# Kernel optimization log

Measured on AMD Instinct MI355X. Metric: run time of the kernel, lower is better.

## Reference

```python
import jax, jax.numpy as jnp
import numpy as np
import math

LMAX = 8
NUM_VECTORS = 64
N_COEF = (LMAX + 1) * (LMAX + 2) // 2  # 45 even-order SH coefficients


def _dfact(n):
    out = 1.0
    k = n
    while k > 1:
        out *= k
        k -= 2
    return out


def sh_tournier_all(xyz, lmax=LMAX):
    """Real even-order spherical harmonics, orders 0,2,...,lmax concatenated
    (m = -l..l within each order), with the Tournier (-1)^|m| sign applied and
    the input permuted xyz -> yzx and normalized (as in the torch module).
    Output: xyz.shape[:-1] + (45,). Fully polynomial in the unit vector, so it
    is smooth/differentiable (no atan2 / division by sin(theta))."""
    yzx = xyz[..., jnp.array([1, 2, 0])]
    r = jnp.sqrt(jnp.sum(yzx * yzx, axis=-1, keepdims=True) + 1e-12)
    u = yzx / r
    px, py, pz = u[..., 0], u[..., 1], u[..., 2]
    # A_m = rho^m cos(m*phi), B_m = rho^m sin(m*phi) via Chebyshev-style recurrence
    A = [jnp.ones_like(px)]
    Bv = [jnp.zeros_like(px)]
    for m in range(1, lmax + 1):
        A.append(px * A[-1] - py * Bv[-1])
        Bv.append(px * Bv[-1] + py * A[-2])
    # Q[l,m] = P_l^m / sin^m(theta): polynomial in pz (Condon-Shortley included)
    Q = {}
    for m in range(lmax + 1):
        qmm = ((-1.0) ** m) * _dfact(2 * m - 1)
        Q[(m, m)] = jnp.full_like(pz, qmm)
        if m < lmax:
            Q[(m + 1, m)] = (2 * m + 1) * qmm * pz
        for l in range(m + 2, lmax + 1):
            Q[(l, m)] = ((2 * l - 1) * pz * Q[(l - 1, m)]
                         - (l + m - 1) * Q[(l - 2, m)]) / (l - m)
    blocks = []
    sqrt2 = math.sqrt(2.0)
    for l in range(0, lmax + 1, 2):
        comps = []
        for m in range(-l, l + 1):
            am = abs(m)
            K = math.sqrt((2 * l + 1) / (4 * math.pi)
                          * math.factorial(l - am) / math.factorial(l + am))
            sgn = -1.0 if am % 2 == 1 else 1.0  # Tournier normalization sign
            if m < 0:
                val = sqrt2 * K * Q[(l, am)] * Bv[am]
            elif m == 0:
                val = K * Q[(l, 0)]
            else:
                val = sqrt2 * K * Q[(l, am)] * A[am]
            comps.append(sgn * val)
        blocks.append(jnp.stack(comps, axis=-1))
    return jnp.concatenate(blocks, axis=-1)


def _forward(image, affine, psf_vectors, M_p):
    B, X, Y, Z, C = image.shape
    V = psf_vectors.shape[0]
    img = jnp.transpose(image.reshape(B, -1, C), (0, 2, 1))      # [B,C,N]
    affine_inv = jnp.linalg.inv(affine)                           # [B,X,Y,Z,3,3]
    w = jnp.einsum('vc,bcn->bvn', M_p, img)                       # PSF weights [B,V,N]
    vi = psf_vectors.T                                            # [3,V]
    vi_hat = affine_inv @ vi                                      # [B,X,Y,Z,3,V]
    M_prime = sh_tournier_all(jnp.swapaxes(vi_hat, -1, -2))       # [B,X,Y,Z,V,C]
    # modulation: |A^{-1} v| / det(A^{-1}) per voxel per vector
    mod = (jnp.sqrt(jnp.sum(vi_hat * vi_hat, axis=-2))
           / jnp.linalg.det(affine_inv)[..., None])               # [B,X,Y,Z,V]
    mod = jnp.moveaxis(mod, -1, 1).reshape(B, V, -1)              # [B,V,N]
    w_mod = mod * w                                               # [B,V,N]
    # per-voxel small GEMV: out[b,n,c] = sum_v M_prime[b,n,v,c] * w_mod[b,v,n]
    out = jnp.einsum('bnvc,bvn->bnc', M_prime.reshape(B, -1, V, C), w_mod)
    return out.reshape(image.shape)


def setup_inputs() -> dict:
    key = jax.random.key(0)
    k1, k2, k3 = jax.random.split(key, 3)
    B, X, Y, Z = 1, 32, 32, 32
    image = jax.random.normal(k1, (B, X, Y, Z, N_COEF), dtype=jnp.float32)
    # per-voxel Jacobian field: near-identity so inverse/det are well-conditioned
    affine = (jnp.eye(3, dtype=jnp.float32)
              + 0.1 * jax.random.normal(k2, (B, X, Y, Z, 3, 3), dtype=jnp.float32))
    psf = jax.random.normal(k3, (NUM_VECTORS, 3), dtype=jnp.float32)
    psf = psf / jnp.linalg.norm(psf, axis=-1, keepdims=True)      # unit PSF directions
    M0 = sh_tournier_all(psf)                                     # [V,45]
    M_p = jnp.linalg.pinv(M0.T)                                   # pinv([45,V]) -> [V,45]
    return {"image": image, "affine": affine, "psf_vectors": psf, "M_p": M_p}


def reference(image, affine, psf_vectors, M_p):
    return _forward(image, affine, psf_vectors, M_p)
```

## Files before the change

### kernel.cpp

```cpp
#include <hip/hip_runtime.h>
#include <type_traits>
#include <utility>

#define CDIM   45
#define LMAXX  8
#define WAVES_PB 4
#define VOXPB  64
#define VDIM   64
#define VPT    (VDIM / WAVES_PB)

constexpr double PI_D = 3.14159265358979323846;

constexpr double dfactd(int n){ double o=1.0; for(int k=n;k>1;k-=2) o*=k; return o; }
constexpr double factd (int n){ double o=1.0; for(int k=2;k<=n;++k) o*=k; return o; }
constexpr double csqrtd(double x){
  if(x<=0.0) return 0.0;
  double g = x>1.0 ? x : 1.0;
  for(int i=0;i<200;++i) g = 0.5*(g + x/g);
  return g;
}

struct SHTab {
  float c1[LMAXX+1][LMAXX+1];
  float c2[LMAXX+1][LMAXX+1];
  float qmm[LMAXX+1];
  float qnx[LMAXX+1];
  float CP [LMAXX+1][LMAXX+1];
};

constexpr SHTab makeTab(){
  SHTab t{};
  for(int m=0;m<=LMAXX;++m){
    double q = ((m&1)?-1.0:1.0)*dfactd(2*m-1);
    t.qmm[m]=(float)q;
    t.qnx[m]=(float)((2.0*m+1.0)*q);
    for(int l=m+2;l<=LMAXX;++l){
      t.c1[m][l]=(float)((2.0*l-1.0)/(double)(l-m));
      t.c2[m][l]=(float)((double)(l+m-1)/(double)(l-m));
    }
    for(int l=m;l<=LMAXX;++l){
      double K = csqrtd((2.0*l+1.0)/(4.0*PI_D)*factd(l-m)/factd(l+m));
      double v = (m==0)? K : (((m&1)?-1.0:1.0)*csqrtd(2.0)*K);
      t.CP[m][l]=(float)v;
    }
  }
  return t;
}
constexpr SHTab SHT = makeTab();

constexpr int offL(int l){ return l==0?0 : (l==2?1 : (l==4?6 : (l==6?15 : 28))); }

template<int N, typename F>
__device__ __forceinline__ void cunroll(F&& f){
  if constexpr (N > 0){
    cunroll<N-1>(f);
    f(std::integral_constant<int, N-1>{});
  }
}

__global__ __launch_bounds__(256, 2)
void fodf_reorient_kernel(const float* __restrict__ image,
                          const float* __restrict__ affine,
                          const float* __restrict__ psf,
                          const float* __restrict__ Mp,
                          float* __restrict__ out,
                          int Nvox)
{
  __shared__ float red[WAVES_PB][VOXPB][CDIM+3];

  const int tid  = threadIdx.x;
  const int lane = tid & 63;
  const int wvi  = __builtin_amdgcn_readfirstlane(tid >> 6);
  const int voxBase = blockIdx.x * VOXPB;
  const int vox  = voxBase + lane;
  const bool valid = vox < Nvox;

  float img[CDIM];
  if (valid){
    const float* ip = image + (long long)vox * CDIM;
    #pragma unroll
    for(int c=0;c<CDIM;++c) img[c] = ip[c];
  } else {
    #pragma unroll
    for(int c=0;c<CDIM;++c) img[c] = 0.0f;
  }

  float a[9];
  if (valid){
    const float* ap = affine + (long long)vox * 9;
    #pragma unroll
    for(int i=0;i<9;++i) a[i] = ap[i];
  } else {
    #pragma unroll
    for(int i=0;i<9;++i) a[i] = (i%4==0) ? 1.0f : 0.0f;
  }

  const float det = a[0]*(a[4]*a[8]-a[5]*a[7])
                  - a[1]*(a[3]*a[8]-a[5]*a[6])
                  + a[2]*(a[3]*a[7]-a[4]*a[6]);
  const float rdet = 1.0f/det;
  const float i00 =  (a[4]*a[8]-a[5]*a[7])*rdet;
  const float i01 = -(a[1]*a[8]-a[2]*a[7])*rdet;
  const float i02 =  (a[1]*a[5]-a[2]*a[4])*rdet;
  const float i10 = -(a[3]*a[8]-a[5]*a[6])*rdet;
  const float i11 =  (a[0]*a[8]-a[2]*a[6])*rdet;
  const float i12 = -(a[0]*a[5]-a[2]*a[3])*rdet;
  const float i20 =  (a[3]*a[7]-a[4]*a[6])*rdet;
  const float i21 = -(a[0]*a[7]-a[1]*a[6])*rdet;
  const float i22 =  (a[0]*a[4]-a[1]*a[3])*rdet;

  float acc[CDIM];
  #pragma unroll
  for(int c=0;c<CDIM;++c) acc[c]=0.0f;

  const int vbase = wvi * VPT;
  #pragma unroll 2
  for(int k=0;k<VPT;++k){
    const int v = vbase + k;
    const float sxv = psf[3*v+0];
    const float syv = psf[3*v+1];
    const float szv = psf[3*v+2];

    const float hx = fmaf(i00,sxv, fmaf(i01,syv, i02*szv));
    const float hy = fmaf(i10,sxv, fmaf(i11,syv, i12*szv));
    const float hz = fmaf(i20,sxv, fmaf(i21,syv, i22*szv));

    const float r2  = fmaf(hx,hx, fmaf(hy,hy, hz*hz));
    const float r2e = r2 + 1e-12f;
    float rin = rsqrtf(r2e);
    rin = rin * (1.5f - 0.5f*r2e*rin*rin);
    const float px = hy*rin;
    const float py = hz*rin;
    const float pz = hx*rin;

    const float modv = sqrtf(r2) * det;

    const float* Mrow = Mp + v*CDIM;
    float w0=0.f,w1=0.f,w2=0.f,w3=0.f;
    #pragma unroll
    for(int c=0;c<44;c+=4){
      w0 = fmaf(Mrow[c+0], img[c+0], w0);
      w1 = fmaf(Mrow[c+1], img[c+1], w1);
      w2 = fmaf(Mrow[c+2], img[c+2], w2);
      w3 = fmaf(Mrow[c+3], img[c+3], w3);
    }
    w0 = fmaf(Mrow[44], img[44], w0);
    const float wval = (w0+w1)+(w2+w3);
    const float wmod = modv * wval;

    float Aa[LMAXX+1], Bb[LMAXX+1];
    Aa[0]=1.0f; Bb[0]=0.0f;
    cunroll<LMAXX>([&](auto Mc){
      constexpr int M = decltype(Mc)::value + 1;
      Aa[M] = fmaf(px, Aa[M-1], -(py*Bb[M-1]));
      Bb[M] = fmaf(px, Bb[M-1],  (py*Aa[M-1]));
    });

    cunroll<LMAXX+1>([&](auto AMc){
      constexpr int AM = decltype(AMc)::value;
      const float fa = wmod * Aa[AM];
      const float fb = wmod * Bb[AM];
      float qp2 = SHT.qmm[AM];
      float qp1 = SHT.qnx[AM]*pz;

      if constexpr ((AM&1)==0){
        constexpr float C = SHT.CP[AM][AM];
        const float t = qp2 * C;
        if constexpr (AM==0){
          acc[0] = fmaf(t, wmod, acc[0]);
        } else {
          acc[offL(AM)+2*AM] = fmaf(t, fa, acc[offL(AM)+2*AM]);
          acc[offL(AM)+0   ] = fmaf(t, fb, acc[offL(AM)+0   ]);
        }
      }
      if constexpr (AM<LMAXX && (((AM+1)&1)==0)){
        constexpr int L = AM+1;
        constexpr float C = SHT.CP[AM][L];
        const float t = qp1 * C;
        acc[offL(L)+L+AM] = fmaf(t, fa, acc[offL(L)+L+AM]);
        acc[offL(L)+L-AM] = fmaf(t, fb, acc[offL(L)+L-AM]);
      }

      constexpr int CNT = (LMAXX-AM-1) > 0 ? (LMAXX-AM-1) : 0;
      cunroll<CNT>([&](auto Lc){
        constexpr int L = AM + 2 + decltype(Lc)::value;
        constexpr float C1 = SHT.c1[AM][L];
        constexpr float C2 = SHT.c2[AM][L];
        const float q = fmaf(C1*pz, qp1, -(C2*qp2));
        qp2 = qp1; qp1 = q;
        if constexpr ((L&1)==0){
          constexpr float C = SHT.CP[AM][L];
          const float t = q * C;
          if constexpr (AM==0){
            acc[offL(L)+L] = fmaf(t, wmod, acc[offL(L)+L]);
          } else {
            acc[offL(L)+L+AM] = fmaf(t, fa, acc[offL(L)+L+AM]);
            acc[offL(L)+L-AM] = fmaf(t, fb, acc[offL(L)+L-AM]);
          }
        }
      });
    });
  }

  #pragma unroll
  for(int c=0;c<CDIM;++c) red[wvi][lane][c] = acc[c];
  __syncthreads();

  const int total = VOXPB * CDIM;
  for(int i = tid; i < total; i += 256){
    const int vx = i / CDIM;
    if (voxBase + vx < Nvox){
      const int c = i - vx*CDIM;
      const float s = red[0][vx][c] + red[1][vx][c]
                    + red[2][vx][c] + red[3][vx][c];
      out[(long long)voxBase*CDIM + i] = s;
    }
  }
}

extern "C" void kernel_launch(void* const* d_in, const int* in_sizes, int n_in,
                              void* d_out, int out_size, void* d_ws, size_t ws_size,
                              hipStream_t stream)
{
  const float* image  = (const float*)d_in[0];
  const float* affine = (const float*)d_in[1];
  const float* psf    = (const float*)d_in[2];
  const float* Mp     = (const float*)d_in[3];
  float* out = (float*)d_out;

  const int Nvox = in_sizes[0] / CDIM;
  const int blocks = (Nvox + VOXPB - 1) / VOXPB;

  hipLaunchKernelGGL(fodf_reorient_kernel, dim3(blocks), dim3(256), 0, stream,
                     image, affine, psf, Mp, out, Nvox);
}
```

Baseline: 80.73 us.

## Double waves per block, reduce via shared atomics, and trim register use

Raises waves per block from 4 to 8 and changes launch bounds to (512, 4), so each wave handles fewer PSF vectors and occupancy rises. The per-wave shared buffer and summation pass are replaced by one zeroed tile that all waves update with LDS atomicAdd. Register pressure is lowered by computing the A/B Chebyshev terms on the fly, dropping the Newton refinement of rsqrt, and setting the vector loop to unroll 1. The costs are atomic contention in LDS, slightly lower rsqrt accuracy, and clamped loads for out-of-range voxels.

```diff
diff --git a/kernel.cpp b/kernel.cpp
--- a/kernel.cpp
+++ b/kernel.cpp
@@ -4,10 +4,11 @@
 
 #define CDIM   45
 #define LMAXX  8
-#define WAVES_PB 4
+#define WAVES_PB 8
 #define VOXPB  64
 #define VDIM   64
 #define VPT    (VDIM / WAVES_PB)
+#define BLOCK  (WAVES_PB * 64)
 
 constexpr double PI_D = 3.14159265358979323846;
 
@@ -58,7 +59,7 @@
   }
 }
 
-__global__ __launch_bounds__(256, 2)
+__global__ __launch_bounds__(BLOCK, 4)
 void fodf_reorient_kernel(const float* __restrict__ image,
                           const float* __restrict__ affine,
                           const float* __restrict__ psf,
@@ -66,33 +67,30 @@
                           float* __restrict__ out,
                           int Nvox)
 {
-  __shared__ float red[WAVES_PB][VOXPB][CDIM+3];
+  __shared__ float red[VOXPB][CDIM+1];
 
   const int tid  = threadIdx.x;
   const int lane = tid & 63;
   const int wvi  = __builtin_amdgcn_readfirstlane(tid >> 6);
   const int voxBase = blockIdx.x * VOXPB;
-  const int vox  = voxBase + lane;
-  const bool valid = vox < Nvox;
+  int vox = voxBase + lane;
+  if (vox >= Nvox) vox = Nvox - 1;
+
+  #pragma unroll 1
+  for (int i = tid; i < VOXPB*(CDIM+1); i += BLOCK) (&red[0][0])[i] = 0.0f;
+  __syncthreads();
 
   float img[CDIM];
-  if (valid){
-    const float* ip = image + (long long)vox * CDIM;
+  {
+    const float* ip = image + (size_t)vox * CDIM;
     #pragma unroll
     for(int c=0;c<CDIM;++c) img[c] = ip[c];
-  } else {
-    #pragma unroll
-    for(int c=0;c<CDIM;++c) img[c] = 0.0f;
-  }
-
+  }
   float a[9];
-  if (valid){
-    const float* ap = affine + (long long)vox * 9;
+  {
+    const float* ap = affine + (size_t)vox * 9;
     #pragma unroll
     for(int i=0;i<9;++i) a[i] = ap[i];
-  } else {
-    #pragma unroll
-    for(int i=0;i<9;++i) a[i] = (i%4==0) ? 1.0f : 0.0f;
   }
 
   const float det = a[0]*(a[4]*a[8]-a[5]*a[7])
@@ -114,7 +112,7 @@
   for(int c=0;c<CDIM;++c) acc[c]=0.0f;
 
   const int vbase = wvi * VPT;
-  #pragma unroll 2
+  #pragma unroll 1
   for(int k=0;k<VPT;++k){
     const int v = vbase + k;
     const float sxv = psf[3*v+0];
@@ -126,14 +124,10 @@
     const float hz = fmaf(i20,sxv, fmaf(i21,syv, i22*szv));
 
     const float r2  = fmaf(hx,hx, fmaf(hy,hy, hz*hz));
-    const float r2e = r2 + 1e-12f;
-    float rin = rsqrtf(r2e);
-    rin = rin * (1.5f - 0.5f*r2e*rin*rin);
+    const float rin = rsqrtf(r2 + 1e-12f);
     const float px = hy*rin;
     const float py = hz*rin;
     const float pz = hx*rin;
-
-    const float modv = sqrtf(r2) * det;
 
     const float* Mrow = Mp + v*CDIM;
     float w0=0.f,w1=0.f,w2=0.f,w3=0.f;
@@ -146,20 +140,19 @@
     }
     w0 = fmaf(Mrow[44], img[44], w0);
     const float wval = (w0+w1)+(w2+w3);
-    const float wmod = modv * wval;
-
-    float Aa[LMAXX+1], Bb[LMAXX+1];
-    Aa[0]=1.0f; Bb[0]=0.0f;
-    cunroll<LMAXX>([&](auto Mc){
-      constexpr int M = decltype(Mc)::value + 1;
-      Aa[M] = fmaf(px, Aa[M-1], -(py*Bb[M-1]));
-      Bb[M] = fmaf(px, Bb[M-1],  (py*Aa[M-1]));
-    });
-
+    const float wmod = r2 * rin * det * wval;
+
+    float Ap = 1.0f, Bp = 0.0f;
     cunroll<LMAXX+1>([&](auto AMc){
       constexpr int AM = decltype(AMc)::value;
-      const float fa = wmod * Aa[AM];
-      const float fb = wmod * Bb[AM];
+      float Acur, Bcur;
+      if constexpr (AM==0){ Acur = 1.0f; Bcur = 0.0f; }
+      else {
+        Acur = fmaf(px, Ap, -(py*Bp));
+        Bcur = fmaf(px, Bp,  (py*Ap));
+      }
+      const float fa = (AM==0) ? wmod : wmod*Acur;
+      const float fb = wmod*Bcur;
       float qp2 = SHT.qmm[AM];
       float qp1 = SHT.qnx[AM]*pz;
 
@@ -199,22 +192,22 @@
           }
         }
       });
+
+      Ap = Acur; Bp = Bcur;
     });
   }
 
   #pragma unroll
-  for(int c=0;c<CDIM;++c) red[wvi][lane][c] = acc[c];
+  for(int c=0;c<CDIM;++c) atomicAdd(&red[lane][c], acc[c]);
   __syncthreads();
 
   const int total = VOXPB * CDIM;
-  for(int i = tid; i < total; i += 256){
+  #pragma unroll 1
+  for(int i = tid; i < total; i += BLOCK){
     const int vx = i / CDIM;
-    if (voxBase + vx < Nvox){
-      const int c = i - vx*CDIM;
-      const float s = red[0][vx][c] + red[1][vx][c]
-                    + red[2][vx][c] + red[3][vx][c];
-      out[(long long)voxBase*CDIM + i] = s;
-    }
+    const int c  = i - vx*CDIM;
+    if (voxBase + vx < Nvox)
+      out[(size_t)voxBase*CDIM + i] = red[vx][c];
   }
 }
 
@@ -231,6 +224,6 @@
   const int Nvox = in_sizes[0] / CDIM;
   const int blocks = (Nvox + VOXPB - 1) / VOXPB;
 
-  hipLaunchKernelGGL(fodf_reorient_kernel, dim3(blocks), dim3(256), 0, stream,
+  hipLaunchKernelGGL(fodf_reorient_kernel, dim3(blocks), dim3(BLOCK), 0, stream,
                      image, affine, psf, Mp, out, Nvox);
 }
```

Result: slower. 187.8 us (+132.6%).
